# Optimization experiments

Measured on AMD Instinct MI355X. Metric: run time of the kernel, lower is better.

Reference implementation:

```python
import jax, jax.numpy as jnp
import numpy as np

N = 50000      # nodes
E = 800000     # edges
IN = 128       # in_ch
OUT = 32       # out_ch
H = 4          # heads
ED = 16        # edge_dim
SLOPE = 0.2    # LeakyReLU negative slope (GATv2 default and outer activation)


def setup_inputs() -> dict:
    key = jax.random.key(0)
    ks = jax.random.split(key, 10)
    s_in = 1.0 / np.sqrt(IN)
    s_ed = 1.0 / np.sqrt(ED)
    s_out = 1.0 / np.sqrt(OUT)
    return {
        "x": jax.random.normal(ks[0], (N, IN), jnp.float32),
        "edge_index": jax.random.randint(ks[1], (2, E), 0, N, dtype=jnp.int32),
        "edges_attr": jax.random.normal(ks[2], (E, ED), jnp.float32),
        "W_l": jax.random.normal(ks[3], (IN, H * OUT), jnp.float32) * s_in,
        "b_l": jnp.zeros((H * OUT,), jnp.float32),
        "W_r": jax.random.normal(ks[4], (IN, H * OUT), jnp.float32) * s_in,
        "b_r": jnp.zeros((H * OUT,), jnp.float32),
        "W_e": jax.random.normal(ks[5], (ED, H * OUT), jnp.float32) * s_ed,
        "att": jax.random.normal(ks[6], (H, OUT), jnp.float32) * s_out,
        "bias": jnp.zeros((OUT,), jnp.float32),
    }


def reference(x, edge_index, edges_attr, W_l, b_l, W_r, b_r, W_e, att, bias):
    src, tgt = edge_index[0], edge_index[1]

    # add_self_loops with fill_value='mean': self-loop attr = scatter-mean of
    # incoming edge attrs per target node (0 for isolated nodes, as in PyG).
    deg = jax.ops.segment_sum(jnp.ones((E,), x.dtype), tgt, num_segments=N)
    attr_sum = jax.ops.segment_sum(edges_attr, tgt, num_segments=N)
    loop_attr = attr_sum / jnp.maximum(deg, 1.0)[:, None]
    node_ids = jnp.arange(N, dtype=src.dtype)
    src_f = jnp.concatenate([src, node_ids])   # [E+N]
    tgt_f = jnp.concatenate([tgt, node_ids])   # [E+N]
    attr_f = jnp.concatenate([edges_attr, loop_attr], axis=0)  # [E+N, ED]

    x_l = (x @ W_l + b_l).reshape(N, H, OUT)   # source transform
    x_r = (x @ W_r + b_r).reshape(N, H, OUT)   # target transform
    e = (attr_f @ W_e).reshape(-1, H, OUT)     # edge transform

    # GATv2 score: att . leaky_relu(x_l[j] + x_r[i] + e_ij)
    m = x_l[src_f] + x_r[tgt_f] + e                          # [E+N, H, OUT]
    scores = jnp.einsum('ehc,hc->eh', jax.nn.leaky_relu(m, SLOPE), att)

    # scatter-softmax over edges grouped by target node (every segment has a
    # self-loop, so segment_max is well-defined)
    smax = jax.ops.segment_max(scores, tgt_f, num_segments=N)
    ex = jnp.exp(scores - smax[tgt_f])
    denom = jax.ops.segment_sum(ex, tgt_f, num_segments=N)
    alpha = ex / denom[tgt_f]                                # [E+N, H]

    # weighted aggregation of source messages x_l[j]
    msg = alpha[:, :, None] * x_l[src_f]                     # [E+N, H, OUT]
    out = jax.ops.segment_sum(msg, tgt_f, num_segments=N)   # [N, H, OUT]

    out = out.mean(axis=1) + bias                            # concat=False -> head mean
    return jax.nn.leaky_relu(out, SLOPE)                     # outer LeakyReLU(0.2)
```

## Files before the change

### kernel.cpp

```cpp
#include <hip/hip_runtime.h>
#include <math.h>

#define NN 50000
#define NE 800000
#define SLOPE 0.2f
#define NB 49
#define GEMMB 782
#define EDGEB 3125


__device__ __forceinline__ void gemm_body(int bx, const float* __restrict__ x,
                                          const float* __restrict__ W,
                                          const float* __restrict__ bptr,
                                          float* __restrict__ optr,
                                          float* xs, float* wsm) {
  int tid = threadIdx.x;
  int cx = tid & 31;
  int rn = tid >> 5;
  int n0 = bx * 64;

  float acc[8][4];
#pragma unroll
  for (int i = 0; i < 8; ++i)
#pragma unroll
    for (int j = 0; j < 4; ++j) acc[i][j] = 0.f;

  for (int kb = 0; kb < 128; kb += 64) {
#pragma unroll
    for (int r = 0; r < 4; ++r) {
      int q = tid + r * 256;
      int n = q >> 4, k4 = q & 15;
      float4 v = make_float4(0.f, 0.f, 0.f, 0.f);
      int gn = n0 + n;
      if (gn < NN) v = *(const float4*)(x + (size_t)gn * 128 + kb + 4 * k4);
      *(float4*)&xs[n * 68 + 4 * k4] = v;
    }
#pragma unroll
    for (int r = 0; r < 8; ++r) {
      int q = tid + r * 256;
      int kk = q >> 5, c4 = q & 31;
      float4 wv = *(const float4*)(W + (size_t)(kb + kk) * 128 + 4 * c4);
      *(float4*)&wsm[kk * 128 + 4 * c4] = wv;
    }
    __syncthreads();
#pragma unroll 2
    for (int k4 = 0; k4 < 16; ++k4) {
      float4 wv[4];
#pragma unroll
      for (int kk = 0; kk < 4; ++kk)
        wv[kk] = *(const float4*)&wsm[(4 * k4 + kk) * 128 + 4 * cx];
#pragma unroll
      for (int i = 0; i < 8; ++i) {
        float4 xv = *(const float4*)&xs[(8 * rn + i) * 68 + 4 * k4];
        acc[i][0] = fmaf(xv.x, wv[0].x, acc[i][0]);
        acc[i][1] = fmaf(xv.x, wv[0].y, acc[i][1]);
        acc[i][2] = fmaf(xv.x, wv[0].z, acc[i][2]);
        acc[i][3] = fmaf(xv.x, wv[0].w, acc[i][3]);
        acc[i][0] = fmaf(xv.y, wv[1].x, acc[i][0]);
        acc[i][1] = fmaf(xv.y, wv[1].y, acc[i][1]);
        acc[i][2] = fmaf(xv.y, wv[1].z, acc[i][2]);
        acc[i][3] = fmaf(xv.y, wv[1].w, acc[i][3]);
        acc[i][0] = fmaf(xv.z, wv[2].x, acc[i][0]);
        acc[i][1] = fmaf(xv.z, wv[2].y, acc[i][1]);
        acc[i][2] = fmaf(xv.z, wv[2].z, acc[i][2]);
        acc[i][3] = fmaf(xv.z, wv[2].w, acc[i][3]);
        acc[i][0] = fmaf(xv.w, wv[3].x, acc[i][0]);
        acc[i][1] = fmaf(xv.w, wv[3].y, acc[i][1]);
        acc[i][2] = fmaf(xv.w, wv[3].z, acc[i][2]);
        acc[i][3] = fmaf(xv.w, wv[3].w, acc[i][3]);
      }
    }
    __syncthreads();
  }

  int cc = 4 * cx;
  float4 bv = *(const float4*)(bptr + cc);
#pragma unroll
  for (int i = 0; i < 8; ++i) {
    int gn = n0 + 8 * rn + i;
    if (gn < NN) {
      float4 o = make_float4(acc[i][0] + bv.x, acc[i][1] + bv.y,
                             acc[i][2] + bv.z, acc[i][3] + bv.w);
      *(float4*)(optr + (size_t)gn * 128 + cc) = o;
    }
  }
}


__launch_bounds__(256)
__global__ void fusedA_kernel(const float* __restrict__ x,
                              const float* __restrict__ W_l, const float* __restrict__ b_l,
                              float* __restrict__ x_l,
                              const int* __restrict__ tgt, int* __restrict__ deg) {
  __shared__ float xs[64 * 68];
  __shared__ float wsm[64 * 128];
  if (blockIdx.x < GEMMB) {
    gemm_body(blockIdx.x, x, W_l, b_l, x_l, xs, wsm);
  } else {
    int e = (blockIdx.x - GEMMB) * 256 + threadIdx.x;
    if (e < NE) atomicAdd(&deg[tgt[e]], 1);
  }
}


__launch_bounds__(256)
__global__ void fusedB_kernel(const float* __restrict__ x,
                              const float* __restrict__ W_r, const float* __restrict__ b_r,
                              float* __restrict__ x_r,
                              const int* __restrict__ src, const int* __restrict__ tgt,
                              const float4* __restrict__ eattr4,
                              int* __restrict__ cursor, int* __restrict__ csr_src,
                              float4* __restrict__ eattr_csr4) {
  __shared__ float xs[64 * 68];
  __shared__ float wsm[64 * 128];
  if (blockIdx.x < GEMMB) {
    gemm_body(blockIdx.x, x, W_r, b_r, x_r, xs, wsm);
  } else {
    int e = (blockIdx.x - GEMMB) * 256 + threadIdx.x;
    if (e < NE) {
      int t = tgt[e];
      float4 a0 = eattr4[(size_t)e * 4 + 0];
      float4 a1 = eattr4[(size_t)e * 4 + 1];
      float4 a2 = eattr4[(size_t)e * 4 + 2];
      float4 a3 = eattr4[(size_t)e * 4 + 3];
      int pos = atomicAdd(&cursor[t], 1);
      csr_src[pos] = src[e];
      eattr_csr4[(size_t)pos * 4 + 0] = a0;
      eattr_csr4[(size_t)pos * 4 + 1] = a1;
      eattr_csr4[(size_t)pos * 4 + 2] = a2;
      eattr_csr4[(size_t)pos * 4 + 3] = a3;
    }
  }
}


__global__ void partial_kernel(const int* __restrict__ deg, int* __restrict__ psum) {
  int b = blockIdx.x;
  int base = b * 1024 + threadIdx.x * 4;
  int s = 0;
  if (base + 3 < NN) {
    int4 v = *(const int4*)(deg + base);
    s = v.x + v.y + v.z + v.w;
  } else {
#pragma unroll
    for (int i = 0; i < 4; ++i)
      if (base + i < NN) s += deg[base + i];
  }
  s += __shfl_xor(s, 1);
  s += __shfl_xor(s, 2);
  s += __shfl_xor(s, 4);
  s += __shfl_xor(s, 8);
  s += __shfl_xor(s, 16);
  s += __shfl_xor(s, 32);
  __shared__ int wsum[4];
  if ((threadIdx.x & 63) == 0) wsum[threadIdx.x >> 6] = s;
  __syncthreads();
  if (threadIdx.x == 0) psum[b] = wsum[0] + wsum[1] + wsum[2] + wsum[3];
}

__global__ void scanpart_kernel(const int* __restrict__ psum, int* __restrict__ offs,
                                int* __restrict__ rowptr) {
  int lane = threadIdx.x;
  int mine = (lane < NB) ? psum[lane] : 0;
  int v = mine;
#pragma unroll
  for (int off = 1; off < 64; off <<= 1) {
    int u = __shfl_up(v, off);
    if (lane >= off) v += u;
  }
  if (lane < NB) offs[lane] = v - mine;
  if (lane == 63) rowptr[NN] = v;
}

__global__ void final_kernel(const int* __restrict__ deg, const int* __restrict__ offs,
                             int* __restrict__ rowptr, int* __restrict__ cursor) {
  int b = blockIdx.x;
  int t = threadIdx.x;
  int base = b * 1024 + t * 4;
  int d0 = 0, d1 = 0, d2 = 0, d3 = 0;
  if (base + 3 < NN) {
    int4 v = *(const int4*)(deg + base);
    d0 = v.x; d1 = v.y; d2 = v.z; d3 = v.w;
  } else {
    if (base < NN) d0 = deg[base];
    if (base + 1 < NN) d1 = deg[base + 1];
    if (base + 2 < NN) d2 = deg[base + 2];
  }
  int s = d0 + d1 + d2 + d3;
  int lane = t & 63, w = t >> 6;
  int v = s;
#pragma unroll
  for (int off = 1; off < 64; off <<= 1) {
    int u = __shfl_up(v, off);
    if (lane >= off) v += u;
  }
  __shared__ int wtot[4];
  if (lane == 63) wtot[w] = v;
  __syncthreads();
  int woff = 0;
#pragma unroll
  for (int i = 0; i < 4; ++i)
    if (i < w) woff += wtot[i];
  int run = offs[b] + woff + (v - s);
  if (base < NN)     { rowptr[base] = run;     cursor[base] = run;     run += d0; }
  if (base + 1 < NN) { rowptr[base + 1] = run; cursor[base + 1] = run; run += d1; }
  if (base + 2 < NN) { rowptr[base + 2] = run; cursor[base + 2] = run; run += d2; }
  if (base + 3 < NN) { rowptr[base + 3] = run; cursor[base + 3] = run; }
}


#define EDGE_PROC(AV, XL)                                              \
  {                                                                    \
    float e0 = AV[0] * wek[0].x;                                       \
    e0 = fmaf(AV[1], wek[1].x, e0);   e0 = fmaf(AV[2], wek[2].x, e0);  \
    e0 = fmaf(AV[3], wek[3].x, e0);   e0 = fmaf(AV[4], wek[4].x, e0);  \
    e0 = fmaf(AV[5], wek[5].x, e0);   e0 = fmaf(AV[6], wek[6].x, e0);  \
    e0 = fmaf(AV[7], wek[7].x, e0);   e0 = fmaf(AV[8], wek[8].x, e0);  \
    e0 = fmaf(AV[9], wek[9].x, e0);   e0 = fmaf(AV[10], wek[10].x, e0);\
    e0 = fmaf(AV[11], wek[11].x, e0); e0 = fmaf(AV[12], wek[12].x, e0);\
    e0 = fmaf(AV[13], wek[13].x, e0); e0 = fmaf(AV[14], wek[14].x, e0);\
    e0 = fmaf(AV[15], wek[15].x, e0);                                  \
    float e1 = AV[0] * wek[0].y;                                       \
    e1 = fmaf(AV[1], wek[1].y, e1);   e1 = fmaf(AV[2], wek[2].y, e1);  \
    e1 = fmaf(AV[3], wek[3].y, e1);   e1 = fmaf(AV[4], wek[4].y, e1);  \
    e1 = fmaf(AV[5], wek[5].y, e1);   e1 = fmaf(AV[6], wek[6].y, e1);  \
    e1 = fmaf(AV[7], wek[7].y, e1);   e1 = fmaf(AV[8], wek[8].y, e1);  \
    e1 = fmaf(AV[9], wek[9].y, e1);   e1 = fmaf(AV[10], wek[10].y, e1);\
    e1 = fmaf(AV[11], wek[11].y, e1); e1 = fmaf(AV[12], wek[12].y, e1);\
    e1 = fmaf(AV[13], wek[13].y, e1); e1 = fmaf(AV[14], wek[14].y, e1);\
    e1 = fmaf(AV[15], wek[15].y, e1);                                  \
    es0 += e0; es1 += e1;                                              \
    float m0 = (XL.x + xr.x) + e0;                                     \
    float m1 = (XL.y + xr.y) + e1;                                     \
    float lm0 = fmaf(SLOPE, fminf(m0, 0.f), fmaxf(m0, 0.f));           \
    float lm1 = fmaf(SLOPE, fminf(m1, 0.f), fmaxf(m1, 0.f));           \
    float part = fmaf(attv.y, lm1, attv.x * lm0);                      \
    part += __shfl_xor(part, 1);                                       \
    part += __shfl_xor(part, 2);                                       \
    part += __shfl_xor(part, 4);                                       \
    part += __shfl_xor(part, 8);                                       \
    float p = __expf(part);                                            \
    lh += p;                                                           \
    acc0 = fmaf(p, XL.x, acc0);                                        \
    acc1 = fmaf(p, XL.y, acc1);                                        \
  }

__launch_bounds__(256)
__global__ void gat_kernel(const float* __restrict__ x_l, const float* __restrict__ x_r,
                           const int* __restrict__ rowptr, const int* __restrict__ csr_src,
                           const float* __restrict__ eattr_csr, const float* __restrict__ W_e,
                           const float* __restrict__ att, const float* __restrict__ bias,
                           float* __restrict__ out) {
  int wid = threadIdx.x >> 6;
  int lane = threadIdx.x & 63;
  int tbase = (blockIdx.x * 4 + wid) * 4;

  float2 wek[16];
#pragma unroll
  for (int k = 0; k < 16; ++k)
    wek[k] = *(const float2*)(W_e + k * 128 + 2 * lane);
  float2 attv = *(const float2*)(att + 2 * lane);
  float bv = bias[(2 * lane) & 31];
  float bv1 = bias[((2 * lane) & 31) + 1];

  for (int tt = 0; tt < 4; ++tt) {
    int t = tbase + tt;
    float2 xr = *(const float2*)(x_r + (size_t)t * 128 + 2 * lane);
    int start = __builtin_amdgcn_readfirstlane(rowptr[t]);
    int end = __builtin_amdgcn_readfirstlane(rowptr[t + 1]);

    float lh = 0.f, acc0 = 0.f, acc1 = 0.f, es0 = 0.f, es1 = 0.f;

    int j = start;
    for (; j + 4 <= end; j += 4) {
      int s0 = __builtin_amdgcn_readfirstlane(csr_src[j]);
      int s1 = __builtin_amdgcn_readfirstlane(csr_src[j + 1]);
      int s2 = __builtin_amdgcn_readfirstlane(csr_src[j + 2]);
      int s3 = __builtin_amdgcn_readfirstlane(csr_src[j + 3]);
      float2 xl0 = *(const float2*)(x_l + (size_t)s0 * 128 + 2 * lane);
      float2 xl1 = *(const float2*)(x_l + (size_t)s1 * 128 + 2 * lane);
      float2 xl2 = *(const float2*)(x_l + (size_t)s2 * 128 + 2 * lane);
      float2 xl3 = *(const float2*)(x_l + (size_t)s3 * 128 + 2 * lane);
      const float* ap0 = eattr_csr + (size_t)j * 16;
      {
        float a0[16];
#pragma unroll
        for (int k = 0; k < 16; ++k) a0[k] = ap0[k];
        EDGE_PROC(a0, xl0)
      }
      {
        float a1[16];
#pragma unroll
        for (int k = 0; k < 16; ++k) a1[k] = ap0[16 + k];
        EDGE_PROC(a1, xl1)
      }
      {
        float a2[16];
#pragma unroll
        for (int k = 0; k < 16; ++k) a2[k] = ap0[32 + k];
        EDGE_PROC(a2, xl2)
      }
      {
        float a3[16];
#pragma unroll
        for (int k = 0; k < 16; ++k) a3[k] = ap0[48 + k];
        EDGE_PROC(a3, xl3)
      }
    }
    if (j + 2 <= end) {
      int s0 = __builtin_amdgcn_readfirstlane(csr_src[j]);
      int s1 = __builtin_amdgcn_readfirstlane(csr_src[j + 1]);
      float2 xl0 = *(const float2*)(x_l + (size_t)s0 * 128 + 2 * lane);
      float2 xl1 = *(const float2*)(x_l + (size_t)s1 * 128 + 2 * lane);
      const float* ap0 = eattr_csr + (size_t)j * 16;
      {
        float a0[16];
#pragma unroll
        for (int k = 0; k < 16; ++k) a0[k] = ap0[k];
        EDGE_PROC(a0, xl0)
      }
      {
        float a1[16];
#pragma unroll
        for (int k = 0; k < 16; ++k) a1[k] = ap0[16 + k];
        EDGE_PROC(a1, xl1)
      }
      j += 2;
    }
    if (j < end) {
      int srcn = __builtin_amdgcn_readfirstlane(csr_src[j]);
      const float* ap = eattr_csr + (size_t)j * 16;
      float aC[16];
#pragma unroll
      for (int k = 0; k < 16; ++k) aC[k] = ap[k];
      float2 xlC = *(const float2*)(x_l + (size_t)srcn * 128 + 2 * lane);
      EDGE_PROC(aC, xlC)
    }

    {
      float rdeg = 1.0f / fmaxf((float)(end - start), 1.0f);
      float e0 = es0 * rdeg, e1 = es1 * rdeg;
      float2 xl = *(const float2*)(x_l + (size_t)t * 128 + 2 * lane);
      float m0 = (xl.x + xr.x) + e0;
      float m1 = (xl.y + xr.y) + e1;
      float lm0 = fmaf(SLOPE, fminf(m0, 0.f), fmaxf(m0, 0.f));
      float lm1 = fmaf(SLOPE, fminf(m1, 0.f), fmaxf(m1, 0.f));
      float part = fmaf(attv.y, lm1, attv.x * lm0);
      part += __shfl_xor(part, 1);
      part += __shfl_xor(part, 2);
      part += __shfl_xor(part, 4);
      part += __shfl_xor(part, 8);
      float p = __expf(part);
      lh += p;
      acc0 = fmaf(p, xl.x, acc0);
      acc1 = fmaf(p, xl.y, acc1);
    }

    float inv = 1.0f / lh;
    float v0 = acc0 * inv, v1 = acc1 * inv;
    v0 += __shfl_xor(v0, 16);
    v0 += __shfl_xor(v0, 32);
    v1 += __shfl_xor(v1, 16);
    v1 += __shfl_xor(v1, 32);
    if (lane < 16) {
      float o0 = fmaf(v0, 0.25f, bv);
      float o1 = fmaf(v1, 0.25f, bv1);
      o0 = fmaf(SLOPE, fminf(o0, 0.f), fmaxf(o0, 0.f));
      o1 = fmaf(SLOPE, fminf(o1, 0.f), fmaxf(o1, 0.f));
      *(float2*)(out + (size_t)t * 32 + 2 * lane) = make_float2(o0, o1);
    }
  }
}


extern "C" void kernel_launch(void* const* d_in, const int* in_sizes, int n_in,
                              void* d_out, int out_size, void* d_ws, size_t ws_size,
                              hipStream_t stream) {
  const float* x = (const float*)d_in[0];
  const int* ei = (const int*)d_in[1];
  const float* eattr = (const float*)d_in[2];
  const float* W_l = (const float*)d_in[3];
  const float* b_l = (const float*)d_in[4];
  const float* W_r = (const float*)d_in[5];
  const float* b_r = (const float*)d_in[6];
  const float* W_e = (const float*)d_in[7];
  const float* att = (const float*)d_in[8];
  const float* bias = (const float*)d_in[9];
  float* out = (float*)d_out;

  char* ws = (char*)d_ws;
  int* csr_src = (int*)ws;
  float* eattr_csr = (float*)(ws + 3200000);
  float* x_l = (float*)(ws + 54400000);
  float* x_r = (float*)(ws + 80000000);
  int* deg = (int*)(ws + 105600000);
  int* rowptr = (int*)(ws + 105800000);
  int* cursor = (int*)(ws + 106000016);
  int* psum = (int*)(ws + 106200016);
  int* offs = (int*)(ws + 106200512);

  hipMemsetAsync(deg, 0, NN * sizeof(int), stream);
  fusedA_kernel<<<GEMMB + EDGEB, 256, 0, stream>>>(x, W_l, b_l, x_l, ei + NE, deg);
  partial_kernel<<<NB, 256, 0, stream>>>(deg, psum);
  scanpart_kernel<<<1, 64, 0, stream>>>(psum, offs, rowptr);
  final_kernel<<<NB, 256, 0, stream>>>(deg, offs, rowptr, cursor);
  fusedB_kernel<<<GEMMB + EDGEB, 256, 0, stream>>>(
      x, W_r, b_r, x_r, ei, ei + NE, (const float4*)eattr, cursor, csr_src,
      (float4*)eattr_csr);
  gat_kernel<<<NN / 16, 256, 0, stream>>>(x_l, x_r, rowptr, csr_src, eattr_csr, W_e, att, bias, out);
}
```

Baseline: 336.5 us.

## Record per-edge rank during degree count and fold block-offset scan into final kernel

Measured after the change: 345.9 us. 1.03x slower.

```diff
diff --git a/kernel.cpp b/kernel.cpp
--- a/kernel.cpp
+++ b/kernel.cpp
@@ -91,14 +91,15 @@
 __global__ void fusedA_kernel(const float* __restrict__ x,
                               const float* __restrict__ W_l, const float* __restrict__ b_l,
                               float* __restrict__ x_l,
-                              const int* __restrict__ tgt, int* __restrict__ deg) {
+                              const int* __restrict__ tgt, int* __restrict__ deg,
+                              int* __restrict__ rank) {
   __shared__ float xs[64 * 68];
   __shared__ float wsm[64 * 128];
   if (blockIdx.x < GEMMB) {
     gemm_body(blockIdx.x, x, W_l, b_l, x_l, xs, wsm);
   } else {
     int e = (blockIdx.x - GEMMB) * 256 + threadIdx.x;
-    if (e < NE) atomicAdd(&deg[tgt[e]], 1);
+    if (e < NE) rank[e] = atomicAdd(&deg[tgt[e]], 1);
   }
 }
 
@@ -108,8 +109,10 @@
                               const float* __restrict__ W_r, const float* __restrict__ b_r,
                               float* __restrict__ x_r,
                               const int* __restrict__ src, const int* __restrict__ tgt,
+                              const int* __restrict__ rank,
+                              const int* __restrict__ rowptr,
                               const float4* __restrict__ eattr4,
-                              int* __restrict__ cursor, int* __restrict__ csr_src,
+                              int* __restrict__ csr_src,
                               float4* __restrict__ eattr_csr4) {
   __shared__ float xs[64 * 68];
   __shared__ float wsm[64 * 128];
@@ -119,11 +122,12 @@
     int e = (blockIdx.x - GEMMB) * 256 + threadIdx.x;
     if (e < NE) {
       int t = tgt[e];
+      int r = rank[e];
       float4 a0 = eattr4[(size_t)e * 4 + 0];
       float4 a1 = eattr4[(size_t)e * 4 + 1];
       float4 a2 = eattr4[(size_t)e * 4 + 2];
       float4 a3 = eattr4[(size_t)e * 4 + 3];
-      int pos = atomicAdd(&cursor[t], 1);
+      int pos = rowptr[t] + r;
       csr_src[pos] = src[e];
       eattr_csr4[(size_t)pos * 4 + 0] = a0;
       eattr_csr4[(size_t)pos * 4 + 1] = a1;
@@ -158,24 +162,26 @@
   if (threadIdx.x == 0) psum[b] = wsum[0] + wsum[1] + wsum[2] + wsum[3];
 }
 
-__global__ void scanpart_kernel(const int* __restrict__ psum, int* __restrict__ offs,
-                                int* __restrict__ rowptr) {
-  int lane = threadIdx.x;
-  int mine = (lane < NB) ? psum[lane] : 0;
-  int v = mine;
-#pragma unroll
-  for (int off = 1; off < 64; off <<= 1) {
-    int u = __shfl_up(v, off);
-    if (lane >= off) v += u;
-  }
-  if (lane < NB) offs[lane] = v - mine;
-  if (lane == 63) rowptr[NN] = v;
-}
-
-__global__ void final_kernel(const int* __restrict__ deg, const int* __restrict__ offs,
-                             int* __restrict__ rowptr, int* __restrict__ cursor) {
+__global__ void final_kernel(const int* __restrict__ deg, const int* __restrict__ psum,
+                             int* __restrict__ rowptr) {
+  __shared__ int offs_s;
+  __shared__ int wtot[4];
   int b = blockIdx.x;
   int t = threadIdx.x;
+  if (t < 64) {
+    int lane = t;
+    int mine = (lane < NB) ? psum[lane] : 0;
+    int v = mine;
+#pragma unroll
+    for (int off = 1; off < 64; off <<= 1) {
+      int u = __shfl_up(v, off);
+      if (lane >= off) v += u;
+    }
+    if (lane == b) offs_s = v - mine;
+    if (b == 0 && lane == 63) rowptr[NN] = v;
+  }
+  __syncthreads();
+
   int base = b * 1024 + t * 4;
   int d0 = 0, d1 = 0, d2 = 0, d3 = 0;
   if (base + 3 < NN) {
@@ -194,18 +200,17 @@
     int u = __shfl_up(v, off);
     if (lane >= off) v += u;
   }
-  __shared__ int wtot[4];
   if (lane == 63) wtot[w] = v;
   __syncthreads();
   int woff = 0;
 #pragma unroll
   for (int i = 0; i < 4; ++i)
     if (i < w) woff += wtot[i];
-  int run = offs[b] + woff + (v - s);
-  if (base < NN)     { rowptr[base] = run;     cursor[base] = run;     run += d0; }
-  if (base + 1 < NN) { rowptr[base + 1] = run; cursor[base + 1] = run; run += d1; }
-  if (base + 2 < NN) { rowptr[base + 2] = run; cursor[base + 2] = run; run += d2; }
-  if (base + 3 < NN) { rowptr[base + 3] = run; cursor[base + 3] = run; }
+  int run = offs_s + woff + (v - s);
+  if (base < NN)     { rowptr[base] = run;     run += d0; }
+  if (base + 1 < NN) { rowptr[base + 1] = run; run += d1; }
+  if (base + 2 < NN) { rowptr[base + 2] = run; run += d2; }
+  if (base + 3 < NN) { rowptr[base + 3] = run; }
 }
 
 
@@ -395,17 +400,15 @@
   float* x_r = (float*)(ws + 80000000);
   int* deg = (int*)(ws + 105600000);
   int* rowptr = (int*)(ws + 105800000);
-  int* cursor = (int*)(ws + 106000016);
-  int* psum = (int*)(ws + 106200016);
-  int* offs = (int*)(ws + 106200512);
+  int* rank = (int*)(ws + 106000016);
+  int* psum = (int*)(ws + 109200016);
 
   hipMemsetAsync(deg, 0, NN * sizeof(int), stream);
-  fusedA_kernel<<<GEMMB + EDGEB, 256, 0, stream>>>(x, W_l, b_l, x_l, ei + NE, deg);
+  fusedA_kernel<<<GEMMB + EDGEB, 256, 0, stream>>>(x, W_l, b_l, x_l, ei + NE, deg, rank);
   partial_kernel<<<NB, 256, 0, stream>>>(deg, psum);
-  scanpart_kernel<<<1, 64, 0, stream>>>(psum, offs, rowptr);
-  final_kernel<<<NB, 256, 0, stream>>>(deg, offs, rowptr, cursor);
+  final_kernel<<<NB, 256, 0, stream>>>(deg, psum, rowptr);
   fusedB_kernel<<<GEMMB + EDGEB, 256, 0, stream>>>(
-      x, W_r, b_r, x_r, ei, ei + NE, (const float4*)eattr, cursor, csr_src,
-      (float4*)eattr_csr);
+      x, W_r, b_r, x_r, ei, ei + NE, rank, rowptr, (const float4*)eattr,
+      csr_src, (float4*)eattr_csr);
   gat_kernel<<<NN / 16, 256, 0, stream>>>(x_l, x_r, rowptr, csr_src, eattr_csr, W_e, att, bias, out);
 }
```
